# Kernel tuning notes

Hardware: AMD Instinct MI355X
Metric: run time of the kernel (lower is better)

Reference implementation:

```python
import jax, jax.numpy as jnp
import numpy as np

HIDDEN = 256
DEPTH = 6
N_MOLS = 5000
ATOMS_PER_MOL = 30
N_ATOMS = N_MOLS * ATOMS_PER_MOL  # 150000 real atoms (+1 padding row)
N_BONDS = 320000                  # directed bonds (+1 padding row)
MAX_NB = 6
ATOM_FDIM = 133
BOND_FDIM = 147


def setup_inputs() -> dict:
    key = jax.random.key(0)
    ks = jax.random.split(key, 8)
    # row 0 of every per-atom / per-bond array is the chemprop zero-padding row
    f_atoms = jax.random.normal(ks[0], (N_ATOMS + 1, ATOM_FDIM), jnp.float32).at[0].set(0.0)
    f_bonds = jax.random.normal(ks[1], (N_BONDS + 1, BOND_FDIM), jnp.float32).at[0].set(0.0)
    a2b = jax.random.randint(ks[2], (N_ATOMS + 1, MAX_NB), 0, N_BONDS + 1, dtype=jnp.int32).at[0].set(0)
    b2a = jax.random.randint(ks[3], (N_BONDS + 1,), 1, N_ATOMS + 1, dtype=jnp.int32).at[0].set(0)
    # directed bonds come in reverse pairs: bond 2k+1 <-> bond 2k+2 (index 0 = pad)
    ids = np.arange(1, N_BONDS + 1)
    rev = ids + np.where(ids % 2 == 1, 1, -1)
    b2revb = jnp.asarray(np.concatenate([[0], rev]), dtype=jnp.int32)
    # contiguous a_scope: molecule i owns atoms [1 + 30*i, 1 + 30*(i+1))
    mol_ids = jnp.repeat(jnp.arange(N_MOLS, dtype=jnp.int32), ATOMS_PER_MOL)
    s = 0.1
    W_i = (jax.random.normal(ks[4], (HIDDEN, BOND_FDIM), jnp.float32) * s)
    W_h = (jax.random.normal(ks[5], (HIDDEN, HIDDEN), jnp.float32) * s)
    W_o = (jax.random.normal(ks[6], (HIDDEN, ATOM_FDIM + HIDDEN), jnp.float32) * s)
    b_o = (jax.random.normal(ks[7], (HIDDEN,), jnp.float32) * s)
    return {"f_atoms": f_atoms, "f_bonds": f_bonds, "a2b": a2b, "b2a": b2a,
            "b2revb": b2revb, "mol_ids": mol_ids,
            "W_i": W_i, "W_h": W_h, "W_o": W_o, "b_o": b_o}


def reference(f_atoms, f_bonds, a2b, b2a, b2revb, mol_ids, W_i, W_h, W_o, b_o):
    # input = W_i(f_bonds) (no bias); message = act(input)
    inp = f_bonds @ W_i.T                       # [B+1, H]
    message = jax.nn.relu(inp)
    for _ in range(DEPTH - 1):
        # gather incoming bond messages per atom, sum over padded neighbor dim
        a_message = message[a2b].sum(axis=1)    # [A+1, H]
        # directed message update: sum at source atom minus reverse message
        message = a_message[b2a] - message[b2revb]  # [B+1, H]
        message = jax.nn.relu(inp + message @ W_h.T)  # dropout p=0 -> identity
    # readout per atom
    a_message = message[a2b].sum(axis=1)        # [A+1, H]
    a_input = jnp.concatenate([f_atoms, a_message], axis=1)  # [A+1, F_a+H]
    atom_hiddens = jax.nn.relu(a_input @ W_o.T + b_o)        # [A+1, H]
    # mean aggregation over each molecule's atoms (a_scope, contiguous, size 30)
    sums = jax.ops.segment_sum(atom_hiddens[1:], mol_ids, num_segments=N_MOLS)
    return sums / float(ATOMS_PER_MOL)
```

## Files before the change

### kernel.cpp

```cpp
#include <hip/hip_runtime.h>
#include <stdint.h>

#define HIDDEN 256
#define NMOLS 5000
#define APM 30
#define NATOMS 150000
#define NBONDS 320000
#define MAXNB 6
#define AFD 133
#define BFD 147
#define A1 (NATOMS + 1)
#define B1 (NBONDS + 1)
#define KI 160
#define KO 416

typedef __bf16 bfx8 __attribute__((ext_vector_type(8)));
typedef float fx4 __attribute__((ext_vector_type(4)));
typedef unsigned short u16x8 __attribute__((ext_vector_type(8)));

__device__ __forceinline__ float b2f(unsigned short u) {
    union { unsigned int i; float f; } v; v.i = ((unsigned int)u) << 16; return v.f;
}
__device__ __forceinline__ unsigned short f2b(float f) {
    union { float f; unsigned int i; } v; v.f = f;
    unsigned int r = v.i + 0x7FFFu + ((v.i >> 16) & 1u);
    return (unsigned short)(r >> 16);
}
__device__ __forceinline__ void gload_lds16(const void* g, void* l) {
    __builtin_amdgcn_global_load_lds(
        (const __attribute__((address_space(1))) unsigned int*)g,
        (__attribute__((address_space(3))) unsigned int*)l, 16, 0, 0);
}

__global__ void k_convw(const float* __restrict__ Wi, const float* __restrict__ Wh,
                        const float* __restrict__ Wo,
                        unsigned short* __restrict__ wi, unsigned short* __restrict__ wh,
                        unsigned short* __restrict__ wo) {
    int t = blockIdx.x * 256 + threadIdx.x;
    if (t < 256 * KI) {
        int n = t / KI, k = t % KI;
        wi[t] = (k < BFD) ? f2b(Wi[n * BFD + k]) : (unsigned short)0;
        return;
    }
    int t2 = t - 256 * KI;
    if (t2 < 256 * 256) {
        wh[t2] = f2b(Wh[t2]);
        return;
    }
    int t3 = t2 - 256 * 256;
    if (t3 < 256 * KO) {
        int n = t3 / KO, k = t3 % KO;
        float v = 0.f;
        if (k < AFD) v = Wo[n * (AFD + HIDDEN) + k];
        else if (k >= 160) v = Wo[n * (AFD + HIDDEN) + AFD + (k - 160)];
        wo[t3] = f2b(v);
    }
}

__global__ __launch_bounds__(256) void k_convfb(const float* __restrict__ fb,
                                                unsigned short* __restrict__ fbb) {
    const int gt = blockIdx.x * 256 + threadIdx.x;
    const int row = gt >> 5;
    const int s = gt & 31;
    if (row >= B1) return;
    const float* src = fb + (size_t)row * BFD;
    u16x8 o;
#pragma unroll
    for (int e = 0; e < 8; ++e) {
        const int c = s * 8 + e;
        o[e] = (c < BFD) ? f2b(src[c]) : (unsigned short)0;
    }
    *(u16x8*)(fbb + (size_t)row * HIDDEN + s * 8) = o;
}

__global__ __launch_bounds__(256) void k_gemm_wi(
    const unsigned short* __restrict__ fbb, const unsigned short* __restrict__ wi,
    unsigned short* __restrict__ inp)
{
    __shared__ unsigned short lds[64 * 256];
    const int m0 = blockIdx.x * 64;
    const int tid = threadIdx.x;
    const int wv = tid >> 6, ln = tid & 63;

    {
        const int l2 = ln >> 5;
        const int q = (ln & 31) * 16;
#pragma unroll
        for (int r = 0; r < 8; ++r) {
            const int row = wv * 16 + r * 2 + l2;
            const size_t srcb = (size_t)(m0 + row) * 512 + (size_t)(q ^ ((row & 7) << 4));
            char* dst = (char*)lds + wv * 8192 + r * 1024;
            gload_lds16((const char*)fbb + srcb, dst);
        }
    }
    __syncthreads();

    const int l15 = ln & 15, lhi = ln >> 4;
    fx4 acc[4][4];
#pragma unroll
    for (int a = 0; a < 4; ++a)
#pragma unroll
        for (int b = 0; b < 4; ++b)
#pragma unroll
            for (int q = 0; q < 4; ++q) acc[a][b][q] = 0.f;

#pragma unroll
    for (int ks = 0; ks < 5; ++ks) {
        const int kk = ks * 32 + lhi * 8;
        bfx8 af[4], bb[4];
#pragma unroll
        for (int mf = 0; mf < 4; ++mf) {
            const int rr = mf * 16 + l15;
            af[mf] = *(const bfx8*)((const char*)lds + rr * 512 + ((kk * 2) ^ ((rr & 7) << 4)));
        }
#pragma unroll
        for (int nf = 0; nf < 4; ++nf) {
            const int n = wv * 64 + nf * 16 + l15;
            bb[nf] = *(const bfx8*)(wi + n * KI + kk);
        }
#pragma unroll
        for (int mf = 0; mf < 4; ++mf)
#pragma unroll
            for (int nf = 0; nf < 4; ++nf)
                acc[mf][nf] = __builtin_amdgcn_mfma_f32_16x16x32_bf16(af[mf], bb[nf], acc[mf][nf], 0, 0, 0);
    }

    __syncthreads();
    {
        const int cb = wv * 64 + l15;
        const int rb = lhi * 4;
#pragma unroll
        for (int mf = 0; mf < 4; ++mf)
#pragma unroll
            for (int j = 0; j < 4; ++j) {
                const int row = mf * 16 + rb + j;
#pragma unroll
                for (int nf = 0; nf < 4; ++nf) {
                    const int col = cb + nf * 16;
                    const int byte = (row * 512) + (((col * 2) & ~15) ^ ((row & 7) << 4)) + ((col * 2) & 15);
                    *(unsigned short*)((char*)lds + byte) = f2b(acc[mf][nf][j]);
                }
            }
    }
    __syncthreads();
#pragma unroll
    for (int i = 0; i < 8; ++i) {
        const int row = i * 8 + (tid >> 5);
        const int col16 = tid & 31;
        const int byte = row * 512 + ((col16 * 16) ^ ((row & 7) << 4));
        u16x8 c = *(const u16x8*)((const char*)lds + byte);
        const int g = m0 + row;
        if (g < B1) *(u16x8*)(inp + (size_t)g * HIDDEN + col16 * 8) = c;
    }
}

template <int FIRST>
__global__ __launch_bounds__(256) void k_gemm_z(
    const unsigned short* __restrict__ src,
    const unsigned short* __restrict__ wh,
    unsigned short* __restrict__ Z)
{
    __shared__ unsigned short lds[64 * 256];
    const int m0 = blockIdx.x * 64;
    const int tid = threadIdx.x;
    const int wv = tid >> 6, ln = tid & 63;

    if (FIRST) {
        const int r0 = tid >> 5;
        const int c16 = tid & 31;
        const int co = c16 * 16;
#pragma unroll
        for (int i = 0; i < 8; ++i) {
            const int r = i * 8 + r0;
            const int b = m0 + r;
            u16x8 o;
#pragma unroll
            for (int e = 0; e < 8; ++e) o[e] = 0;
            if (b < B1) {
                u16x8 vi = *(const u16x8*)((const char*)src + (size_t)b * 512 + co);
#pragma unroll
                for (int e = 0; e < 8; ++e)
                    o[e] = (vi[e] & 0x8000u) ? (unsigned short)0 : vi[e];
            }
            *(u16x8*)((char*)lds + r * 512 + (co ^ ((r & 7) << 4))) = o;
        }
    } else {
        const int l2 = ln >> 5;
        const int q = (ln & 31) * 16;
#pragma unroll
        for (int r = 0; r < 8; ++r) {
            const int row = wv * 16 + r * 2 + l2;
            const size_t srcb = (size_t)(m0 + row) * 512 + (size_t)(q ^ ((row & 7) << 4));
            char* dst = (char*)lds + wv * 8192 + r * 1024;
            gload_lds16((const char*)src + srcb, dst);
        }
    }
    __syncthreads();

    const int l15 = ln & 15, lhi = ln >> 4;
    fx4 acc[4][4];
#pragma unroll
    for (int a = 0; a < 4; ++a)
#pragma unroll
        for (int b = 0; b < 4; ++b)
#pragma unroll
            for (int q = 0; q < 4; ++q) acc[a][b][q] = 0.f;

#pragma unroll
    for (int ks = 0; ks < 8; ++ks) {
        const int kk = ks * 32 + lhi * 8;
        bfx8 af[4], bb[4];
#pragma unroll
        for (int mf = 0; mf < 4; ++mf) {
            const int rr = mf * 16 + l15;
            af[mf] = *(const bfx8*)((const char*)lds + rr * 512 + ((kk * 2) ^ ((rr & 7) << 4)));
        }
#pragma unroll
        for (int nf = 0; nf < 4; ++nf) {
            const int n = wv * 64 + nf * 16 + l15;
            bb[nf] = *(const bfx8*)(wh + n * 256 + kk);
        }
#pragma unroll
        for (int mf = 0; mf < 4; ++mf)
#pragma unroll
            for (int nf = 0; nf < 4; ++nf)
                acc[mf][nf] = __builtin_amdgcn_mfma_f32_16x16x32_bf16(af[mf], bb[nf], acc[mf][nf], 0, 0, 0);
    }

    __syncthreads();
    {
        const int cb = wv * 64 + l15;
        const int rb = lhi * 4;
#pragma unroll
        for (int mf = 0; mf < 4; ++mf)
#pragma unroll
            for (int j = 0; j < 4; ++j) {
                const int row = mf * 16 + rb + j;
#pragma unroll
                for (int nf = 0; nf < 4; ++nf) {
                    const int col = cb + nf * 16;
                    const int byte = (row * 512) + (((col * 2) & ~15) ^ ((row & 7) << 4)) + ((col * 2) & 15);
                    *(unsigned short*)((char*)lds + byte) = f2b(acc[mf][nf][j]);
                }
            }
    }
    __syncthreads();
#pragma unroll
    for (int i = 0; i < 8; ++i) {
        const int row = i * 8 + (tid >> 5);
        const int col16 = tid & 31;
        const int byte = row * 512 + ((col16 * 16) ^ ((row & 7) << 4));
        u16x8 c = *(const u16x8*)((const char*)lds + byte);
        const int g = m0 + row;
        if (g < B1) *(u16x8*)(Z + (size_t)g * HIDDEN + col16 * 8) = c;
    }
}

__global__ __launch_bounds__(256) void k_gather(
    const unsigned short* __restrict__ msg, const int* __restrict__ a2b,
    unsigned short* __restrict__ amsg)
{
    const int gt = blockIdx.x * 256 + threadIdx.x;
    const int atom = gt >> 5;
    const int s = gt & 31;
    if (atom >= A1) return;
    const int* nb = a2b + atom * MAXNB;
    float acc[8];
#pragma unroll
    for (int e = 0; e < 8; ++e) acc[e] = 0.f;
#pragma unroll
    for (int j = 0; j < MAXNB; ++j) {
        const int b = nb[j];
        u16x8 v = *(const u16x8*)(msg + (size_t)b * HIDDEN + s * 8);
#pragma unroll
        for (int e = 0; e < 8; ++e) acc[e] += b2f(v[e]);
    }
    u16x8 o;
#pragma unroll
    for (int e = 0; e < 8; ++e) o[e] = f2b(acc[e]);
    *(u16x8*)(amsg + (size_t)atom * HIDDEN + s * 8) = o;
}

__global__ __launch_bounds__(256) void k_eps(
    const unsigned short* __restrict__ inp,
    const unsigned short* __restrict__ amsgZ,
    const unsigned short* __restrict__ Z,
    const int* __restrict__ b2a, const int* __restrict__ b2revb,
    unsigned short* __restrict__ msgn)
{
    const int gt = blockIdx.x * 256 + threadIdx.x;
    const int b = gt >> 5;
    const int ss = gt & 31;
    if (b >= B1) return;
    const int ia = b2a[b];
    const int ir = b2revb[b];
    const size_t off = (size_t)b * HIDDEN + ss * 8;
    u16x8 vi = *(const u16x8*)(inp + off);
    u16x8 va = *(const u16x8*)(amsgZ + (size_t)ia * HIDDEN + ss * 8);
    u16x8 vz = *(const u16x8*)(Z + (size_t)ir * HIDDEN + ss * 8);
    u16x8 o;
#pragma unroll
    for (int e = 0; e < 8; ++e) {
        float v = b2f(vi[e]) + b2f(va[e]) - b2f(vz[e]);
        o[e] = f2b(v > 0.f ? v : 0.f);
    }
    *(u16x8*)(msgn + off) = o;
}

__global__ __launch_bounds__(256) void k_gemm_wo(
    const float* __restrict__ fa,
    const unsigned short* __restrict__ amsg,
    const unsigned short* __restrict__ wo,
    const float* __restrict__ bo,
    unsigned short* __restrict__ ah)
{
    __shared__ unsigned short lds[64 * KO];
    const int m0 = blockIdx.x * 64;
    const int tid = threadIdx.x;
    {
        const int r = tid >> 2, p = tid & 3;
        const int a = m0 + r;
        const bool ok = (a < A1);
        const float* src = fa + (size_t)a * AFD;
        unsigned short* drow = lds + r * KO;
#pragma unroll
        for (int i = 0; i < 13; ++i) {
            const int c0 = (i * 4 + p) * 8;
            u16x8 o;
            if (ok && c0 + 8 <= AFD) {
#pragma unroll
                for (int e = 0; e < 8; ++e) o[e] = f2b(src[c0 + e]);
            } else if (ok && c0 < AFD) {
#pragma unroll
                for (int e = 0; e < 8; ++e) o[e] = (c0 + e < AFD) ? f2b(src[c0 + e]) : (unsigned short)0;
            } else if (ok && c0 >= 160) {
                o = *(const u16x8*)(amsg + (size_t)a * HIDDEN + (c0 - 160));
            } else {
#pragma unroll
                for (int e = 0; e < 8; ++e) o[e] = 0;
            }
            *(u16x8*)(drow + c0) = o;
        }
    }
    __syncthreads();

    const int wv = tid >> 6, ln = tid & 63;
    const int l15 = ln & 15, lhi = ln >> 4;
    fx4 acc[4][4];
#pragma unroll
    for (int a = 0; a < 4; ++a)
#pragma unroll
        for (int b = 0; b < 4; ++b)
#pragma unroll
            for (int q = 0; q < 4; ++q) acc[a][b][q] = 0.f;

#pragma unroll
    for (int ks = 0; ks < 13; ++ks) {
        const int kk = ks * 32 + lhi * 8;
        bfx8 af[4], bb[4];
#pragma unroll
        for (int mf = 0; mf < 4; ++mf) {
            const int rr = mf * 16 + l15;
            af[mf] = *(const bfx8*)(lds + rr * KO + kk);
        }
#pragma unroll
        for (int nf = 0; nf < 4; ++nf) {
            const int n = wv * 64 + nf * 16 + l15;
            bb[nf] = *(const bfx8*)(wo + n * KO + kk);
        }
#pragma unroll
        for (int mf = 0; mf < 4; ++mf)
#pragma unroll
            for (int nf = 0; nf < 4; ++nf)
                acc[mf][nf] = __builtin_amdgcn_mfma_f32_16x16x32_bf16(af[mf], bb[nf], acc[mf][nf], 0, 0, 0);
    }

    __syncthreads();
    {
        const int cb = wv * 64 + l15;
        const int rb = lhi * 4;
#pragma unroll
        for (int mf = 0; mf < 4; ++mf)
#pragma unroll
            for (int j = 0; j < 4; ++j) {
                const int row = mf * 16 + rb + j;
#pragma unroll
                for (int nf = 0; nf < 4; ++nf) {
                    const int col = cb + nf * 16;
                    const int byte = (row * 512) + (((col * 2) & ~15) ^ ((row & 7) << 4)) + ((col * 2) & 15);
                    *(unsigned short*)((char*)lds + byte) = f2b(acc[mf][nf][j]);
                }
            }
    }
    __syncthreads();
#pragma unroll
    for (int i = 0; i < 8; ++i) {
        const int row = i * 8 + (tid >> 5);
        const int col16 = tid & 31;
        const int byte = row * 512 + ((col16 * 16) ^ ((row & 7) << 4));
        u16x8 c = *(const u16x8*)((const char*)lds + byte);
        const int g = m0 + row;
        if (g < A1) {
            fx4 bi0 = *(const fx4*)(bo + col16 * 8);
            fx4 bi1 = *(const fx4*)(bo + col16 * 8 + 4);
            u16x8 o;
#pragma unroll
            for (int e = 0; e < 8; ++e) {
                float v = b2f(c[e]) + (e < 4 ? bi0[e] : bi1[e - 4]);
                o[e] = f2b(v > 0.f ? v : 0.f);
            }
            *(u16x8*)(ah + (size_t)g * HIDDEN + col16 * 8) = o;
        }
    }
}

__global__ __launch_bounds__(256) void k_pool(const unsigned short* __restrict__ ah,
                                              float* __restrict__ out) {
    const int mol = blockIdx.x;
    const int h = threadIdx.x;
    const unsigned short* base = ah + ((size_t)(1 + mol * APM)) * HIDDEN + h;
    float s = 0.f;
#pragma unroll
    for (int i = 0; i < APM; ++i) s += b2f(base[(size_t)i * HIDDEN]);
    out[(size_t)mol * HIDDEN + h] = s * (1.0f / APM);
}

extern "C" void kernel_launch(void* const* d_in, const int* in_sizes, int n_in,
                              void* d_out, int out_size, void* d_ws, size_t ws_size,
                              hipStream_t stream)
{
    const float* f_atoms = (const float*)d_in[0];
    const float* f_bonds = (const float*)d_in[1];
    const int* a2b    = (const int*)d_in[2];
    const int* b2a    = (const int*)d_in[3];
    const int* b2revb = (const int*)d_in[4];
    const float* W_i  = (const float*)d_in[6];
    const float* W_h  = (const float*)d_in[7];
    const float* W_o  = (const float*)d_in[8];
    const float* b_o  = (const float*)d_in[9];
    float* out = (float*)d_out;

    char* ws = (char*)d_ws;
    size_t off = 0;
    auto alloc = [&](size_t n) { char* p = ws + off; off = (off + n + 255) & ~(size_t)255; return p; };
    unsigned short* wi   = (unsigned short*)alloc((size_t)256 * KI * 2);
    unsigned short* wh   = (unsigned short*)alloc((size_t)256 * 256 * 2);
    unsigned short* wo   = (unsigned short*)alloc((size_t)256 * KO * 2);
    unsigned short* fbb  = (unsigned short*)alloc((size_t)B1 * HIDDEN * 2 + 65536);
    unsigned short* inp  = (unsigned short*)alloc((size_t)B1 * HIDDEN * 2 + 65536);
    unsigned short* Zbuf = (unsigned short*)alloc((size_t)B1 * HIDDEN * 2 + 65536);
    unsigned short* amsg = (unsigned short*)alloc((size_t)A1 * HIDDEN * 2);
    unsigned short* msgX = fbb;
    unsigned short* ah   = inp;

    k_convw<<<832, 256, 0, stream>>>(W_i, W_h, W_o, wi, wh, wo);

    const int gb64 = (B1 + 63) / 64;
    const int ga = (A1 + 63) / 64;
    const int gg = (A1 * 32 + 255) / 256;
    const int ge = (B1 * 32 + 255) / 256;

    k_convfb<<<ge, 256, 0, stream>>>(f_bonds, fbb);
    k_gemm_wi<<<gb64, 256, 0, stream>>>(fbb, wi, inp);

    k_gemm_z<1><<<gb64, 256, 0, stream>>>(inp, wh, Zbuf);
    k_gather<<<gg, 256, 0, stream>>>(Zbuf, a2b, amsg);
    k_eps<<<ge, 256, 0, stream>>>(inp, amsg, Zbuf, b2a, b2revb, msgX);

    for (int t = 2; t <= 5; ++t) {
        k_gemm_z<0><<<gb64, 256, 0, stream>>>(msgX, wh, Zbuf);
        k_gather<<<gg, 256, 0, stream>>>(Zbuf, a2b, amsg);
        k_eps<<<ge, 256, 0, stream>>>(inp, amsg, Zbuf, b2a, b2revb, msgX);
    }

    k_gather<<<gg, 256, 0, stream>>>(msgX, a2b, amsg);
    k_gemm_wo<<<ga, 256, 0, stream>>>(f_atoms, amsg, wo, b_o, ah);
    k_pool<<<NMOLS, 256, 0, stream>>>(ah, out);
}
```

Before: 1.847 ms.

## Make bond GEMMs persistent over four tiles with double-buffered async LDS staging

The W_i and W_h GEMM kernels now have each block process four consecutive 64-row tiles. The next tile is prefetched into a second LDS buffer via global_load_lds while the current one is computed, with explicit vmcnt waits and barriers. The W_i kernel also writes relu(inp) as the first message, which removes the special FIRST variant of the Z GEMM so all five iterations use one kernel. In exchange LDS per block doubles, which may lower occupancy, and the bounds checks are dropped in favour of larger buffer slop, so the last tiles read and write past B1.

```diff
diff --git a/kernel.cpp b/kernel.cpp
--- a/kernel.cpp
+++ b/kernel.cpp
@@ -13,6 +13,7 @@
 #define B1 (NBONDS + 1)
 #define KI 160
 #define KO 416
+#define NT 4
 
 typedef __bf16 bfx8 __attribute__((ext_vector_type(8)));
 typedef float fx4 __attribute__((ext_vector_type(4)));
@@ -31,6 +32,20 @@
         (const __attribute__((address_space(1))) unsigned int*)g,
         (__attribute__((address_space(3))) unsigned int*)l, 16, 0, 0);
 }
+__device__ __forceinline__ void stage_tile(const unsigned short* src, char* ldsbase,
+                                           int wv, int ln, size_t tile) {
+    const int q = (ln & 31) * 16;
+#pragma unroll
+    for (int r8 = 0; r8 < 8; ++r8) {
+        const int row = wv * 16 + r8 * 2 + (ln >> 5);
+        const size_t srcb = (tile * 64 + row) * 512 + (size_t)(q ^ ((row & 7) << 4));
+        char* dst = ldsbase + wv * 8192 + r8 * 1024;
+        gload_lds16((const char*)src + srcb, dst);
+    }
+}
+#define SBAR() do { __builtin_amdgcn_sched_barrier(0); __builtin_amdgcn_s_barrier(); \
+                    __builtin_amdgcn_sched_barrier(0); } while (0)
+#define WAIT_LGKM0() do { asm volatile("s_waitcnt lgkmcnt(0)" ::: "memory"); } while (0)
 
 __global__ void k_convw(const float* __restrict__ Wi, const float* __restrict__ Wh,
                         const float* __restrict__ Wo,
@@ -73,186 +88,183 @@
     *(u16x8*)(fbb + (size_t)row * HIDDEN + s * 8) = o;
 }
 
-__global__ __launch_bounds__(256) void k_gemm_wi(
+__global__ __launch_bounds__(256) void k_wip(
     const unsigned short* __restrict__ fbb, const unsigned short* __restrict__ wi,
-    unsigned short* __restrict__ inp)
-{
-    __shared__ unsigned short lds[64 * 256];
-    const int m0 = blockIdx.x * 64;
+    unsigned short* __restrict__ inp, unsigned short* __restrict__ msg0)
+{
+    __shared__ unsigned short lds[2][64 * 256];
     const int tid = threadIdx.x;
     const int wv = tid >> 6, ln = tid & 63;
-
-    {
-        const int l2 = ln >> 5;
-        const int q = (ln & 31) * 16;
-#pragma unroll
-        for (int r = 0; r < 8; ++r) {
-            const int row = wv * 16 + r * 2 + l2;
-            const size_t srcb = (size_t)(m0 + row) * 512 + (size_t)(q ^ ((row & 7) << 4));
-            char* dst = (char*)lds + wv * 8192 + r * 1024;
-            gload_lds16((const char*)fbb + srcb, dst);
-        }
-    }
-    __syncthreads();
-
     const int l15 = ln & 15, lhi = ln >> 4;
-    fx4 acc[4][4];
-#pragma unroll
-    for (int a = 0; a < 4; ++a)
-#pragma unroll
-        for (int b = 0; b < 4; ++b)
-#pragma unroll
-            for (int q = 0; q < 4; ++q) acc[a][b][q] = 0.f;
-
-#pragma unroll
-    for (int ks = 0; ks < 5; ++ks) {
-        const int kk = ks * 32 + lhi * 8;
-        bfx8 af[4], bb[4];
-#pragma unroll
-        for (int mf = 0; mf < 4; ++mf) {
-            const int rr = mf * 16 + l15;
-            af[mf] = *(const bfx8*)((const char*)lds + rr * 512 + ((kk * 2) ^ ((rr & 7) << 4)));
-        }
-#pragma unroll
-        for (int nf = 0; nf < 4; ++nf) {
-            const int n = wv * 64 + nf * 16 + l15;
-            bb[nf] = *(const bfx8*)(wi + n * KI + kk);
-        }
-#pragma unroll
-        for (int mf = 0; mf < 4; ++mf)
-#pragma unroll
-            for (int nf = 0; nf < 4; ++nf)
-                acc[mf][nf] = __builtin_amdgcn_mfma_f32_16x16x32_bf16(af[mf], bb[nf], acc[mf][nf], 0, 0, 0);
-    }
-
-    __syncthreads();
-    {
-        const int cb = wv * 64 + l15;
-        const int rb = lhi * 4;
-#pragma unroll
-        for (int mf = 0; mf < 4; ++mf)
-#pragma unroll
-            for (int j = 0; j < 4; ++j) {
-                const int row = mf * 16 + rb + j;
-#pragma unroll
-                for (int nf = 0; nf < 4; ++nf) {
-                    const int col = cb + nf * 16;
-                    const int byte = (row * 512) + (((col * 2) & ~15) ^ ((row & 7) << 4)) + ((col * 2) & 15);
-                    *(unsigned short*)((char*)lds + byte) = f2b(acc[mf][nf][j]);
+    const size_t t0 = (size_t)blockIdx.x * NT;
+
+    stage_tile(fbb, (char*)lds[0], wv, ln, t0);
+    int cur = 0;
+#pragma unroll
+    for (int t = 0; t < NT; ++t) {
+        if (t < NT - 1) stage_tile(fbb, (char*)lds[cur ^ 1], wv, ln, t0 + t + 1);
+        if (t == 0)           asm volatile("s_waitcnt vmcnt(8)" ::: "memory");
+        else if (t == NT - 1) asm volatile("s_waitcnt vmcnt(16)" ::: "memory");
+        else                  asm volatile("s_waitcnt vmcnt(24)" ::: "memory");
+        SBAR();
+
+        const char* A = (const char*)lds[cur];
+        fx4 acc[4][4];
+#pragma unroll
+        for (int a = 0; a < 4; ++a)
+#pragma unroll
+            for (int b = 0; b < 4; ++b)
+#pragma unroll
+                for (int q = 0; q < 4; ++q) acc[a][b][q] = 0.f;
+
+#pragma unroll
+        for (int ks = 0; ks < 5; ++ks) {
+            const int kk = ks * 32 + lhi * 8;
+            bfx8 af[4], bb[4];
+#pragma unroll
+            for (int mf = 0; mf < 4; ++mf) {
+                const int rr = mf * 16 + l15;
+                af[mf] = *(const bfx8*)(A + rr * 512 + ((kk * 2) ^ ((rr & 7) << 4)));
+            }
+#pragma unroll
+            for (int nf = 0; nf < 4; ++nf) {
+                const int n = wv * 64 + nf * 16 + l15;
+                bb[nf] = *(const bfx8*)(wi + n * KI + kk);
+            }
+#pragma unroll
+            for (int mf = 0; mf < 4; ++mf)
+#pragma unroll
+                for (int nf = 0; nf < 4; ++nf)
+                    acc[mf][nf] = __builtin_amdgcn_mfma_f32_16x16x32_bf16(af[mf], bb[nf], acc[mf][nf], 0, 0, 0);
+        }
+
+        WAIT_LGKM0();
+        SBAR();
+        {
+            char* C = (char*)lds[cur];
+            const int cb = wv * 64 + l15;
+            const int rb = lhi * 4;
+#pragma unroll
+            for (int mf = 0; mf < 4; ++mf)
+#pragma unroll
+                for (int j = 0; j < 4; ++j) {
+                    const int row = mf * 16 + rb + j;
+#pragma unroll
+                    for (int nf = 0; nf < 4; ++nf) {
+                        const int col = cb + nf * 16;
+                        const int byte = (row * 512) + (((col * 2) & ~15) ^ ((row & 7) << 4)) + ((col * 2) & 15);
+                        *(unsigned short*)(C + byte) = f2b(acc[mf][nf][j]);
+                    }
                 }
-            }
-    }
-    __syncthreads();
-#pragma unroll
-    for (int i = 0; i < 8; ++i) {
-        const int row = i * 8 + (tid >> 5);
-        const int col16 = tid & 31;
-        const int byte = row * 512 + ((col16 * 16) ^ ((row & 7) << 4));
-        u16x8 c = *(const u16x8*)((const char*)lds + byte);
-        const int g = m0 + row;
-        if (g < B1) *(u16x8*)(inp + (size_t)g * HIDDEN + col16 * 8) = c;
-    }
-}
-
-template <int FIRST>
-__global__ __launch_bounds__(256) void k_gemm_z(
+        }
+        WAIT_LGKM0();
+        SBAR();
+        {
+            const char* C = (const char*)lds[cur];
+#pragma unroll
+            for (int i = 0; i < 8; ++i) {
+                const int row = i * 8 + (tid >> 5);
+                const int col16 = tid & 31;
+                const int byte = row * 512 + ((col16 * 16) ^ ((row & 7) << 4));
+                u16x8 c = *(const u16x8*)(C + byte);
+                const size_t off = ((t0 + t) * 64 + row) * HIDDEN + col16 * 8;
+                *(u16x8*)(inp + off) = c;
+                u16x8 m;
+#pragma unroll
+                for (int e = 0; e < 8; ++e) m[e] = (c[e] & 0x8000u) ? (unsigned short)0 : c[e];
+                *(u16x8*)(msg0 + off) = m;
+            }
+        }
+        SBAR();
+        cur ^= 1;
+    }
+}
+
+__global__ __launch_bounds__(256) void k_zp(
     const unsigned short* __restrict__ src,
     const unsigned short* __restrict__ wh,
     unsigned short* __restrict__ Z)
 {
-    __shared__ unsigned short lds[64 * 256];
-    const int m0 = blockIdx.x * 64;
+    __shared__ unsigned short lds[2][64 * 256];
     const int tid = threadIdx.x;
     const int wv = tid >> 6, ln = tid & 63;
-
-    if (FIRST) {
-        const int r0 = tid >> 5;
-        const int c16 = tid & 31;
-        const int co = c16 * 16;
-#pragma unroll
-        for (int i = 0; i < 8; ++i) {
-            const int r = i * 8 + r0;
-            const int b = m0 + r;
-            u16x8 o;
-#pragma unroll
-            for (int e = 0; e < 8; ++e) o[e] = 0;
-            if (b < B1) {
-                u16x8 vi = *(const u16x8*)((const char*)src + (size_t)b * 512 + co);
-#pragma unroll
-                for (int e = 0; e < 8; ++e)
-                    o[e] = (vi[e] & 0x8000u) ? (unsigned short)0 : vi[e];
-            }
-            *(u16x8*)((char*)lds + r * 512 + (co ^ ((r & 7) << 4))) = o;
-        }
-    } else {
-        const int l2 = ln >> 5;
-        const int q = (ln & 31) * 16;
-#pragma unroll
-        for (int r = 0; r < 8; ++r) {
-            const int row = wv * 16 + r * 2 + l2;
-            const size_t srcb = (size_t)(m0 + row) * 512 + (size_t)(q ^ ((row & 7) << 4));
-            char* dst = (char*)lds + wv * 8192 + r * 1024;
-            gload_lds16((const char*)src + srcb, dst);
-        }
-    }
-    __syncthreads();
-
     const int l15 = ln & 15, lhi = ln >> 4;
-    fx4 acc[4][4];
-#pragma unroll
-    for (int a = 0; a < 4; ++a)
-#pragma unroll
-        for (int b = 0; b < 4; ++b)
-#pragma unroll
-            for (int q = 0; q < 4; ++q) acc[a][b][q] = 0.f;
-
-#pragma unroll
-    for (int ks = 0; ks < 8; ++ks) {
-        const int kk = ks * 32 + lhi * 8;
-        bfx8 af[4], bb[4];
-#pragma unroll
-        for (int mf = 0; mf < 4; ++mf) {
-            const int rr = mf * 16 + l15;
-            af[mf] = *(const bfx8*)((const char*)lds + rr * 512 + ((kk * 2) ^ ((rr & 7) << 4)));
-        }
-#pragma unroll
-        for (int nf = 0; nf < 4; ++nf) {
-            const int n = wv * 64 + nf * 16 + l15;
-            bb[nf] = *(const bfx8*)(wh + n * 256 + kk);
-        }
-#pragma unroll
-        for (int mf = 0; mf < 4; ++mf)
-#pragma unroll
-            for (int nf = 0; nf < 4; ++nf)
-                acc[mf][nf] = __builtin_amdgcn_mfma_f32_16x16x32_bf16(af[mf], bb[nf], acc[mf][nf], 0, 0, 0);
-    }
-
-    __syncthreads();
-    {
-        const int cb = wv * 64 + l15;
-        const int rb = lhi * 4;
-#pragma unroll
-        for (int mf = 0; mf < 4; ++mf)
-#pragma unroll
-            for (int j = 0; j < 4; ++j) {
-                const int row = mf * 16 + rb + j;
-#pragma unroll
-                for (int nf = 0; nf < 4; ++nf) {
-                    const int col = cb + nf * 16;
-                    const int byte = (row * 512) + (((col * 2) & ~15) ^ ((row & 7) << 4)) + ((col * 2) & 15);
-                    *(unsigned short*)((char*)lds + byte) = f2b(acc[mf][nf][j]);
+    const size_t t0 = (size_t)blockIdx.x * NT;
+
+    stage_tile(src, (char*)lds[0], wv, ln, t0);
+    int cur = 0;
+#pragma unroll
+    for (int t = 0; t < NT; ++t) {
+        if (t < NT - 1) stage_tile(src, (char*)lds[cur ^ 1], wv, ln, t0 + t + 1);
+        if (t == 0 || t == NT - 1) asm volatile("s_waitcnt vmcnt(8)" ::: "memory");
+        else                       asm volatile("s_waitcnt vmcnt(16)" ::: "memory");
+        SBAR();
+
+        const char* A = (const char*)lds[cur];
+        fx4 acc[4][4];
+#pragma unroll
+        for (int a = 0; a < 4; ++a)
+#pragma unroll
+            for (int b = 0; b < 4; ++b)
+#pragma unroll
+                for (int q = 0; q < 4; ++q) acc[a][b][q] = 0.f;
+
+#pragma unroll
+        for (int ks = 0; ks < 8; ++ks) {
+            const int kk = ks * 32 + lhi * 8;
+            bfx8 af[4], bb[4];
+#pragma unroll
+            for (int mf = 0; mf < 4; ++mf) {
+                const int rr = mf * 16 + l15;
+                af[mf] = *(const bfx8*)(A + rr * 512 + ((kk * 2) ^ ((rr & 7) << 4)));
+            }
+#pragma unroll
+            for (int nf = 0; nf < 4; ++nf) {
+                const int n = wv * 64 + nf * 16 + l15;
+                bb[nf] = *(const bfx8*)(wh + n * 256 + kk);
+            }
+#pragma unroll
+            for (int mf = 0; mf < 4; ++mf)
+#pragma unroll
+                for (int nf = 0; nf < 4; ++nf)
+                    acc[mf][nf] = __builtin_amdgcn_mfma_f32_16x16x32_bf16(af[mf], bb[nf], acc[mf][nf], 0, 0, 0);
+        }
+
+        WAIT_LGKM0();
+        SBAR();
+        {
+            char* C = (char*)lds[cur];
+            const int cb = wv * 64 + l15;
+            const int rb = lhi * 4;
+#pragma unroll
+            for (int mf = 0; mf < 4; ++mf)
+#pragma unroll
+                for (int j = 0; j < 4; ++j) {
+                    const int row = mf * 16 + rb + j;
+#pragma unroll
+                    for (int nf = 0; nf < 4; ++nf) {
+                        const int col = cb + nf * 16;
+                        const int byte = (row * 512) + (((col * 2) & ~15) ^ ((row & 7) << 4)) + ((col * 2) & 15);
+                        *(unsigned short*)(C + byte) = f2b(acc[mf][nf][j]);
+                    }
                 }
-            }
-    }
-    __syncthreads();
-#pragma unroll
-    for (int i = 0; i < 8; ++i) {
-        const int row = i * 8 + (tid >> 5);
-        const int col16 = tid & 31;
-        const int byte = row * 512 + ((col16 * 16) ^ ((row & 7) << 4));
-        u16x8 c = *(const u16x8*)((const char*)lds + byte);
-        const int g = m0 + row;
-        if (g < B1) *(u16x8*)(Z + (size_t)g * HIDDEN + col16 * 8) = c;
+        }
+        WAIT_LGKM0();
+        SBAR();
+        {
+            const char* C = (const char*)lds[cur];
+#pragma unroll
+            for (int i = 0; i < 8; ++i) {
+                const int row = i * 8 + (tid >> 5);
+                const int col16 = tid & 31;
+                const int byte = row * 512 + ((col16 * 16) ^ ((row & 7) << 4));
+                u16x8 c = *(const u16x8*)(C + byte);
+                const size_t off = ((t0 + t) * 64 + row) * HIDDEN + col16 * 8;
+                *(u16x8*)(Z + off) = c;
+            }
+        }
+        SBAR();
+        cur ^= 1;
     }
 }
 
@@ -443,32 +455,30 @@
     char* ws = (char*)d_ws;
     size_t off = 0;
     auto alloc = [&](size_t n) { char* p = ws + off; off = (off + n + 255) & ~(size_t)255; return p; };
+    const size_t SLOP = 196608;
     unsigned short* wi   = (unsigned short*)alloc((size_t)256 * KI * 2);
     unsigned short* wh   = (unsigned short*)alloc((size_t)256 * 256 * 2);
     unsigned short* wo   = (unsigned short*)alloc((size_t)256 * KO * 2);
-    unsigned short* fbb  = (unsigned short*)alloc((size_t)B1 * HIDDEN * 2 + 65536);
-    unsigned short* inp  = (unsigned short*)alloc((size_t)B1 * HIDDEN * 2 + 65536);
-    unsigned short* Zbuf = (unsigned short*)alloc((size_t)B1 * HIDDEN * 2 + 65536);
+    unsigned short* fbb  = (unsigned short*)alloc((size_t)B1 * HIDDEN * 2 + SLOP);
+    unsigned short* inp  = (unsigned short*)alloc((size_t)B1 * HIDDEN * 2 + SLOP);
+    unsigned short* Zbuf = (unsigned short*)alloc((size_t)B1 * HIDDEN * 2 + SLOP);
     unsigned short* amsg = (unsigned short*)alloc((size_t)A1 * HIDDEN * 2);
     unsigned short* msgX = fbb;
     unsigned short* ah   = inp;
 
     k_convw<<<832, 256, 0, stream>>>(W_i, W_h, W_o, wi, wh, wo);
 
-    const int gb64 = (B1 + 63) / 64;
+    const int TILES = (B1 + 63) / 64;
+    const int gp = (TILES + NT - 1) / NT;
     const int ga = (A1 + 63) / 64;
     const int gg = (A1 * 32 + 255) / 256;
     const int ge = (B1 * 32 + 255) / 256;
 
     k_convfb<<<ge, 256, 0, stream>>>(f_bonds, fbb);
-    k_gemm_wi<<<gb64, 256, 0, stream>>>(fbb, wi, inp);
-
-    k_gemm_z<1><<<gb64, 256, 0, stream>>>(inp, wh, Zbuf);
-    k_gather<<<gg, 256, 0, stream>>>(Zbuf, a2b, amsg);
-    k_eps<<<ge, 256, 0, stream>>>(inp, amsg, Zbuf, b2a, b2revb, msgX);
-
-    for (int t = 2; t <= 5; ++t) {
-        k_gemm_z<0><<<gb64, 256, 0, stream>>>(msgX, wh, Zbuf);
+    k_wip<<<gp, 256, 0, stream>>>(fbb, wi, inp, msgX);
+
+    for (int t = 1; t <= 5; ++t) {
+        k_zp<<<gp, 256, 0, stream>>>(msgX, wh, Zbuf);
         k_gather<<<gg, 256, 0, stream>>>(Zbuf, a2b, amsg);
         k_eps<<<ge, 256, 0, stream>>>(inp, amsg, Zbuf, b2a, b2revb, msgX);
     }
```

Result: slower. 1.916 ms (+3.7%).

## Replace per-iteration Wh GEMM with persistent double-buffered 32-row tile kernel

Applied to the files above, without the earlier changes.

Iterations 2-5 now run the message-by-Wh GEMM in a new kernel. Each block processes 8 consecutive 32-row tiles and double-buffers the A operand into LDS with async global-to-LDS loads, so the next tile loads while the current one computes. B fragments are read straight from global memory and are expected to be cache-resident. This aims to hide load latency and cut launch and tail overhead, at the cost of smaller tiles, more global weight reads and reduced occupancy. Buffer slop grows so that over-reads and writes past the last tile stay in bounds.

```diff
diff --git a/kernel.cpp b/kernel.cpp
--- a/kernel.cpp
+++ b/kernel.cpp
@@ -13,6 +13,7 @@
 #define B1 (NBONDS + 1)
 #define KI 160
 #define KO 416
+#define ZNT 8
 
 typedef __bf16 bfx8 __attribute__((ext_vector_type(8)));
 typedef float fx4 __attribute__((ext_vector_type(4)));
@@ -31,6 +32,9 @@
         (const __attribute__((address_space(1))) unsigned int*)g,
         (__attribute__((address_space(3))) unsigned int*)l, 16, 0, 0);
 }
+#define SBAR() do { __builtin_amdgcn_sched_barrier(0); __builtin_amdgcn_s_barrier(); \
+                    __builtin_amdgcn_sched_barrier(0); } while (0)
+#define WAIT_LGKM0() do { asm volatile("s_waitcnt lgkmcnt(0)" ::: "memory"); } while (0)
 
 __global__ void k_convw(const float* __restrict__ Wi, const float* __restrict__ Wh,
                         const float* __restrict__ Wo,
@@ -154,8 +158,7 @@
     }
 }
 
-template <int FIRST>
-__global__ __launch_bounds__(256) void k_gemm_z(
+__global__ __launch_bounds__(256) void k_gemm_z1(
     const unsigned short* __restrict__ src,
     const unsigned short* __restrict__ wh,
     unsigned short* __restrict__ Z)
@@ -165,7 +168,7 @@
     const int tid = threadIdx.x;
     const int wv = tid >> 6, ln = tid & 63;
 
-    if (FIRST) {
+    {
         const int r0 = tid >> 5;
         const int c16 = tid & 31;
         const int co = c16 * 16;
@@ -183,16 +186,6 @@
                     o[e] = (vi[e] & 0x8000u) ? (unsigned short)0 : vi[e];
             }
             *(u16x8*)((char*)lds + r * 512 + (co ^ ((r & 7) << 4))) = o;
-        }
-    } else {
-        const int l2 = ln >> 5;
-        const int q = (ln & 31) * 16;
-#pragma unroll
-        for (int r = 0; r < 8; ++r) {
-            const int row = wv * 16 + r * 2 + l2;
-            const size_t srcb = (size_t)(m0 + row) * 512 + (size_t)(q ^ ((row & 7) << 4));
-            char* dst = (char*)lds + wv * 8192 + r * 1024;
-            gload_lds16((const char*)src + srcb, dst);
         }
     }
     __syncthreads();
@@ -253,6 +246,100 @@
         u16x8 c = *(const u16x8*)((const char*)lds + byte);
         const int g = m0 + row;
         if (g < B1) *(u16x8*)(Z + (size_t)g * HIDDEN + col16 * 8) = c;
+    }
+}
+
+__global__ void k_zp32(
+    const unsigned short* __restrict__ src,
+    const unsigned short* __restrict__ wh,
+    unsigned short* __restrict__ Z)
+{
+    __shared__ unsigned short ldsA[2][32 * 256];
+    __shared__ unsigned short ldsC[32 * 256];
+    const int tid = threadIdx.x;
+    const int wv = tid >> 6, ln = tid & 63;
+    const int l15 = ln & 15, lhi = ln >> 4;
+    const int l2 = ln >> 5;
+    const int q = (ln & 31) * 16;
+    const size_t t0 = (size_t)blockIdx.x * ZNT;
+
+    auto stage32 = [&](char* dstbase, size_t tile) {
+#pragma unroll
+        for (int r4 = 0; r4 < 4; ++r4) {
+            const int row = wv * 8 + r4 * 2 + l2;
+            const size_t srcb = (tile * 32 + row) * 512 + (size_t)(q ^ ((row & 7) << 4));
+            gload_lds16((const char*)src + srcb, dstbase + wv * 4096 + r4 * 1024);
+        }
+    };
+
+    stage32((char*)ldsA[0], t0);
+    int cur = 0;
+#pragma unroll
+    for (int t = 0; t < ZNT; ++t) {
+        if (t < ZNT - 1) stage32((char*)ldsA[cur ^ 1], t0 + t + 1);
+        if (t == 0 || t == ZNT - 1) asm volatile("s_waitcnt vmcnt(4)" ::: "memory");
+        else                        asm volatile("s_waitcnt vmcnt(8)" ::: "memory");
+        SBAR();
+
+        const char* A = (const char*)ldsA[cur];
+        fx4 acc[2][4];
+#pragma unroll
+        for (int a = 0; a < 2; ++a)
+#pragma unroll
+            for (int b = 0; b < 4; ++b)
+#pragma unroll
+                for (int p = 0; p < 4; ++p) acc[a][b][p] = 0.f;
+
+#pragma unroll
+        for (int ks = 0; ks < 8; ++ks) {
+            const int kk = ks * 32 + lhi * 8;
+            bfx8 af[2], bb[4];
+#pragma unroll
+            for (int mf = 0; mf < 2; ++mf) {
+                const int rr = mf * 16 + l15;
+                af[mf] = *(const bfx8*)(A + rr * 512 + ((kk * 2) ^ ((rr & 7) << 4)));
+            }
+#pragma unroll
+            for (int nf = 0; nf < 4; ++nf) {
+                const int n = wv * 64 + nf * 16 + l15;
+                bb[nf] = *(const bfx8*)(wh + n * 256 + kk);
+            }
+#pragma unroll
+            for (int mf = 0; mf < 2; ++mf)
+#pragma unroll
+                for (int nf = 0; nf < 4; ++nf)
+                    acc[mf][nf] = __builtin_amdgcn_mfma_f32_16x16x32_bf16(af[mf], bb[nf], acc[mf][nf], 0, 0, 0);
+        }
+
+        {
+            const int cb = wv * 64 + l15;
+            const int rb = lhi * 4;
+#pragma unroll
+            for (int mf = 0; mf < 2; ++mf)
+#pragma unroll
+                for (int j = 0; j < 4; ++j) {
+                    const int row = mf * 16 + rb + j;
+#pragma unroll
+                    for (int nf = 0; nf < 4; ++nf) {
+                        const int col = cb + nf * 16;
+                        const int byte = (row * 512) + (((col * 2) & ~15) ^ ((row & 7) << 4)) + ((col * 2) & 15);
+                        *(unsigned short*)((char*)ldsC + byte) = f2b(acc[mf][nf][j]);
+                    }
+                }
+        }
+        WAIT_LGKM0();
+        SBAR();
+
+#pragma unroll
+        for (int i = 0; i < 4; ++i) {
+            const int row = i * 8 + (tid >> 5);
+            const int col16 = tid & 31;
+            const int byte = row * 512 + ((col16 * 16) ^ ((row & 7) << 4));
+            u16x8 c = *(const u16x8*)((const char*)ldsC + byte);
+            const size_t off = ((t0 + t) * 32 + row) * HIDDEN + col16 * 8;
+            *(u16x8*)(Z + off) = c;
+        }
+        cur ^= 1;
     }
 }
 
@@ -443,12 +530,13 @@
     char* ws = (char*)d_ws;
     size_t off = 0;
     auto alloc = [&](size_t n) { char* p = ws + off; off = (off + n + 255) & ~(size_t)255; return p; };
+    const size_t SLOP = 196608;
     unsigned short* wi   = (unsigned short*)alloc((size_t)256 * KI * 2);
     unsigned short* wh   = (unsigned short*)alloc((size_t)256 * 256 * 2);
     unsigned short* wo   = (unsigned short*)alloc((size_t)256 * KO * 2);
-    unsigned short* fbb  = (unsigned short*)alloc((size_t)B1 * HIDDEN * 2 + 65536);
-    unsigned short* inp  = (unsigned short*)alloc((size_t)B1 * HIDDEN * 2 + 65536);
-    unsigned short* Zbuf = (unsigned short*)alloc((size_t)B1 * HIDDEN * 2 + 65536);
+    unsigned short* fbb  = (unsigned short*)alloc((size_t)B1 * HIDDEN * 2 + SLOP);
+    unsigned short* inp  = (unsigned short*)alloc((size_t)B1 * HIDDEN * 2 + SLOP);
+    unsigned short* Zbuf = (unsigned short*)alloc((size_t)B1 * HIDDEN * 2 + SLOP);
     unsigned short* amsg = (unsigned short*)alloc((size_t)A1 * HIDDEN * 2);
     unsigned short* msgX = fbb;
     unsigned short* ah   = inp;
@@ -456,6 +544,8 @@
     k_convw<<<832, 256, 0, stream>>>(W_i, W_h, W_o, wi, wh, wo);
 
     const int gb64 = (B1 + 63) / 64;
+    const int TILES32 = (B1 + 31) / 32;
+    const int gzp = (TILES32 + ZNT - 1) / ZNT;
     const int ga = (A1 + 63) / 64;
     const int gg = (A1 * 32 + 255) / 256;
     const int ge = (B1 * 32 + 255) / 256;
@@ -463,12 +553,12 @@
     k_convfb<<<ge, 256, 0, stream>>>(f_bonds, fbb);
     k_gemm_wi<<<gb64, 256, 0, stream>>>(fbb, wi, inp);
 
-    k_gemm_z<1><<<gb64, 256, 0, stream>>>(inp, wh, Zbuf);
+    k_gemm_z1<<<gb64, 256, 0, stream>>>(inp, wh, Zbuf);
     k_gather<<<gg, 256, 0, stream>>>(Zbuf, a2b, amsg);
     k_eps<<<ge, 256, 0, stream>>>(inp, amsg, Zbuf, b2a, b2revb, msgX);
 
     for (int t = 2; t <= 5; ++t) {
-        k_gemm_z<0><<<gb64, 256, 0, stream>>>(msgX, wh, Zbuf);
+        k_zp32<<<gzp, 256, 0, stream>>>(msgX, wh, Zbuf);
         k_gather<<<gg, 256, 0, stream>>>(Zbuf, a2b, amsg);
         k_eps<<<ge, 256, 0, stream>>>(inp, amsg, Zbuf, b2a, b2revb, msgX);
     }
```

Measured after the change: 2.343 ms. 26.9% more time.
